# Kernel tuning notes

Measured on AMD Instinct MI355X. Metric: run time of the kernel, lower is better.

## Reference

```python
import jax, jax.numpy as jnp
import numpy as np

B_, D1, D2, M_, Q_, IC, OC, BATCH = 8, 2, 2, 2, 30, 8, 16, 2
BB = 2 * B_            # 16
MM = 2 * (M_ + 1)      # 6
U = 2 * D1 + 1         # 5
V = 2 * D2 + 1         # 5
NC = U * V             # 25


def collect_weights(coeffs):
    # coeffs: [iC, nCoeffs, oC] real -> W: [iC*nCoeffs, oC] complex
    iC, nC, oC = coeffs.shape
    wZ = coeffs[:, 0, :].astype(jnp.complex64)
    wS = coeffs[:, 1:, :].reshape(iC, (nC - 1) // 2, 2, oC).transpose(0, 1, 3, 2)
    w = wS[..., 0] + 1j * wS[..., 1]
    W = jnp.concatenate([jnp.flip(w, 1), wZ[:, None, :], w], axis=1)
    return W.reshape(-1, oC)


def setup_inputs() -> dict:
    key = jax.random.key(0)
    ks = jax.random.split(key, 17)
    r = lambda k, shp, s: (jax.random.normal(k, shp, dtype=jnp.float32) * s)
    return {
        'x_re': r(ks[0], (BATCH, BB, BB, IC), 1.0),
        'x_im': r(ks[1], (BATCH, BB, BB, IC), 1.0),
        'lnAlpha': r(ks[2], (BATCH, BB, BB, IC), 0.3),
        'Phi': r(ks[3], (BATCH, BB, BB, IC), 1.0),
        'lnTau': r(ks[4], (BATCH, BB, BB, IC), 0.3),
        'Psi': r(ks[5], (BATCH, BB, BB, IC), 1.0),
        'pAlpha_re': r(ks[6], (Q_, MM), 0.5),
        'pAlpha_im': r(ks[7], (Q_, MM), 0.5),
        'pPhi_re': r(ks[8], (1, MM), 0.5),
        'pPhi_im': r(ks[9], (1, MM), 0.5),
        'pTau_re': r(ks[10], (Q_, MM, U, 1), 0.5),
        'pTau_im': r(ks[11], (Q_, MM, U, 1), 0.5),
        'pPsi_re': r(ks[12], (1, MM, 1, V), 0.5),
        'pPsi_im': r(ks[13], (1, MM, 1, V), 0.5),
        'F_re': r(ks[14], (Q_, MM, U, V), 1.0),
        'F_im': r(ks[15], (Q_, MM, U, V), 1.0),
        'coeffs': r(ks[16], (IC, NC, OC), 0.1),
    }


def reference(x_re, x_im, lnAlpha, Phi, lnTau, Psi,
              pAlpha_re, pAlpha_im, pPhi_re, pPhi_im,
              pTau_re, pTau_im, pPsi_re, pPsi_im,
              F_re, F_im, coeffs):
    pAlpha = pAlpha_re + 1j * pAlpha_im        # [Q, MM]
    pPhi = pPhi_re + 1j * pPhi_im              # [1, MM]
    pTau = pTau_re + 1j * pTau_im              # [Q, MM, U, 1]
    pPsi = pPsi_re + 1j * pPsi_im              # [1, MM, 1, V]
    F = F_re + 1j * F_im                       # [Q, MM, U, V]
    x = x_re + 1j * x_im                       # [b, BB, BB, iC]
    iC = x.shape[-1]

    # Laplace/Mellin basis on (alpha, phi): [b, Q, MM, BB, BB, iC]
    A = x[:, None, None] * jnp.exp(
        lnAlpha[:, None, None] * pAlpha[None, :, :, None, None, None]
        + Phi[:, None, None] * pPhi[None, :, :, None, None, None])
    # basis on (tau, psi) with filter taps u, v: [b, Q, MM, BB, BB, iC, U, V]
    E = (lnTau[:, None, None, :, :, :, None, None] * pTau[None, :, :, None, None, None]
         + Psi[:, None, None, :, :, :, None, None] * pPsi[None, :, :, None, None, None])
    G = A[..., None, None] * jnp.exp(E)        # [b, Q, MM, BB, BB, iC, U, V]

    W = collect_weights(coeffs)                # [iC*U*V, oC]
    Wr = W.reshape(iC, U, V, -1)               # [iC, U, V, oC]
    # matmul over flattened (iC, u, v), fused with filter F, then permute (0,5,1,2,3,4)
    out = jnp.einsum('bqmyxcuv,qmuv,cuvo->boqmyx', G, F, Wr)
    # return real/imag stacked so the baseline is real-valued: [b, oC, Q, MM, BB, BB, 2]
    return jnp.stack([out.real, out.imag], axis=-1)
```

## Files before the change

kernel.cpp:

```cpp
#include <hip/hip_runtime.h>
#include <hip/hip_bf16.h>

#define NBATCH 2
#define NBB    16
#define NIC    8
#define NOC    16
#define NQ     30
#define NMM    6
#define NU     5
#define NV     5
#define NNC    25

typedef __attribute__((ext_vector_type(8))) short bf16x8;
typedef __attribute__((ext_vector_type(4))) float f32x4;

__device__ __forceinline__ unsigned pk2(float a, float b) {
    unsigned ua = __builtin_bit_cast(unsigned, a);
    unsigned ub = __builtin_bit_cast(unsigned, b);
    ua += 0x7fffu + ((ua >> 16) & 1u);
    ub += 0x7fffu + ((ub >> 16) & 1u);
    return (ua >> 16) | (ub & 0xffff0000u);
}

__device__ __forceinline__ float2 wentry(const float* __restrict__ coeffs,
                                         int c, int n, int o) {
    if (n < 12)
        return make_float2(coeffs[(c * NNC + (23 - 2 * n)) * NOC + o],
                           coeffs[(c * NNC + (24 - 2 * n)) * NOC + o]);
    if (n == 12)
        return make_float2(coeffs[(c * NNC) * NOC + o], 0.0f);
    return make_float2(coeffs[(c * NNC + (2 * n - 25)) * NOC + o],
                       coeffs[(c * NNC + (2 * n - 24)) * NOC + o]);
}

#define EU_G(U)                                                          \
    const float ru##U = __expf(lt * pTau_re[qm * NU + U]);               \
    float su##U, cu##U;                                                  \
    __sincosf(lt * pTau_im[qm * NU + U], &su##U, &cu##U);                \
    const float g##U##r = Are * (ru##U * cu##U) - Aim * (ru##U * su##U); \
    const float g##U##i = Are * (ru##U * su##U) + Aim * (ru##U * cu##U);

#define EVV(V)                                                           \
    const float rv##V = __expf(ps * pPsi_re[m * NV + V]);                \
    float sv##V, cv##V;                                                  \
    __sincosf(ps * pPsi_im[m * NV + V], &sv##V, &cv##V);                 \
    const float e##V##r = rv##V * cv##V, e##V##i = rv##V * sv##V;

#define TAP(N, U, V)                                                     \
    const float tr##N = g##U##r * e##V##r - g##U##i * e##V##i;           \
    const float ti##N = g##U##r * e##V##i + g##U##i * e##V##r;

#define MT_MFMA(SUF, MT, CH, BWR, BWI) {                                 \
    const bf16x8 atr = *reinterpret_cast<const bf16x8*>(                 \
        &T_lds[(CH) * (128 * 36) + ((MT) * 16 + l15) * 36 + sl * 4]);    \
    const bf16x8 ati = *reinterpret_cast<const bf16x8*>(                 \
        &T_lds[(CH) * (128 * 36) + ((MT) * 16 + l15) * 36 + 16 + sl * 4]);\
    aRR##SUF = __builtin_amdgcn_mfma_f32_16x16x32_bf16(atr, BWR, aRR##SUF, 0, 0, 0); \
    aII##SUF = __builtin_amdgcn_mfma_f32_16x16x32_bf16(ati, BWI, aII##SUF, 0, 0, 0); \
    aRI##SUF = __builtin_amdgcn_mfma_f32_16x16x32_bf16(atr, BWI, aRI##SUF, 0, 0, 0); \
    aIR##SUF = __builtin_amdgcn_mfma_f32_16x16x32_bf16(ati, BWR, aIR##SUF, 0, 0, 0); }

__global__ __launch_bounds__(256, 3) void lbc_main(
    const float* __restrict__ x_re,   const float* __restrict__ x_im,
    const float* __restrict__ lnAlpha,const float* __restrict__ Phi,
    const float* __restrict__ lnTau,  const float* __restrict__ Psi,
    const float* __restrict__ pAlpha_re, const float* __restrict__ pAlpha_im,
    const float* __restrict__ pPhi_re,   const float* __restrict__ pPhi_im,
    const float* __restrict__ pTau_re,   const float* __restrict__ pTau_im,
    const float* __restrict__ pPsi_re,   const float* __restrict__ pPsi_im,
    const float* __restrict__ F_re,      const float* __restrict__ F_im,
    const float* __restrict__ coeffs,
    float* __restrict__ out)
{
    __shared__ unsigned T_lds[2 * 128 * 36];
    __shared__ unsigned W_lds[2 * NIC * 64 * 4];

    const int bid  = blockIdx.x;
    const int half = bid & 1;
    const int rest = bid >> 1;
    const int m    = rest % NMM;
    const int q    = (rest / NMM) % NQ;
    const int b    = rest / (NMM * NQ);
    const int qm   = q * NMM + m;

    for (int idx = threadIdx.x; idx < 2 * NIC * 64 * 4; idx += 256) {
        const int j  = idx & 3;
        const int l  = (idx >> 2) & 63;
        const int c  = (idx >> 8) & 7;
        const int pl = idx >> 11;
        const int o  = l & 15;
        const int k0 = (l >> 4) * 8 + 2 * j;
        float v0 = 0.f, v1 = 0.f;
        if (k0 < NNC) {
            const float2 w = wentry(coeffs, c, k0, o);
            const float fr = F_re[qm * NNC + k0], fi = F_im[qm * NNC + k0];
            v0 = pl ? (w.x * fi + w.y * fr) : (w.x * fr - w.y * fi);
        }
        if (k0 + 1 < NNC) {
            const float2 w = wentry(coeffs, c, k0 + 1, o);
            const float fr = F_re[qm * NNC + k0 + 1], fi = F_im[qm * NNC + k0 + 1];
            v1 = pl ? (w.x * fi + w.y * fr) : (w.x * fr - w.y * fi);
        }
        W_lds[idx] = pk2(v0, v1);
    }

    const int tid = threadIdx.x;
    const int ptl = tid & 127;
    const int h   = tid >> 7;
    const int y   = half * 8 + (ptl >> 4);
    const int x   = ptl & 15;
    const int pbase = ((b * NBB + y) * NBB + x) * NIC;

    const int l   = tid & 63;
    const int w   = tid >> 6;
    const int l15 = l & 15;
    const int sl  = l >> 4;

    const float pAre = pAlpha_re[qm], pAim = pAlpha_im[qm];
    const float pPre = pPhi_re[m],    pPim = pPhi_im[m];

    f32x4 aRRa = {0.f, 0.f, 0.f, 0.f}, aIIa = {0.f, 0.f, 0.f, 0.f};
    f32x4 aRIa = {0.f, 0.f, 0.f, 0.f}, aIRa = {0.f, 0.f, 0.f, 0.f};
    f32x4 aRRb = {0.f, 0.f, 0.f, 0.f}, aIIb = {0.f, 0.f, 0.f, 0.f};
    f32x4 aRIb = {0.f, 0.f, 0.f, 0.f}, aIRb = {0.f, 0.f, 0.f, 0.f};

    __syncthreads();

    #pragma unroll 1
    for (int s = 0; s < 4; ++s) {
        {
            const int c  = h * 4 + s;
            const int pc = pbase + c;
            const float xr = x_re[pc], xi = x_im[pc];
            const float la = lnAlpha[pc], ph = Phi[pc];
            const float lt = lnTau[pc],   ps = Psi[pc];

            const float ar = la * pAre + ph * pPre;
            const float ai = la * pAim + ph * pPim;
            const float ea = __expf(ar);
            float sa, ca;
            __sincosf(ai, &sa, &ca);
            const float er_ = ea * ca, ei_ = ea * sa;
            const float Are = xr * er_ - xi * ei_;
            const float Aim = xr * ei_ + xi * er_;

            EU_G(0) EU_G(1) EU_G(2) EU_G(3) EU_G(4)
            EVV(0) EVV(1) EVV(2) EVV(3) EVV(4)

            uint4* trow = reinterpret_cast<uint4*>(&T_lds[h * (128 * 36) + ptl * 36]);

            {
                TAP(0,0,0) TAP(1,0,1) TAP(2,0,2) TAP(3,0,3)
                TAP(4,0,4) TAP(5,1,0) TAP(6,1,1) TAP(7,1,2)
                trow[0] = make_uint4(pk2(tr0,tr1), pk2(tr2,tr3), pk2(tr4,tr5), pk2(tr6,tr7));
                trow[4] = make_uint4(pk2(ti0,ti1), pk2(ti2,ti3), pk2(ti4,ti5), pk2(ti6,ti7));
            }
            {
                TAP(8,1,3) TAP(9,1,4) TAP(10,2,0) TAP(11,2,1)
                TAP(12,2,2) TAP(13,2,3) TAP(14,2,4) TAP(15,3,0)
                trow[1] = make_uint4(pk2(tr8,tr9), pk2(tr10,tr11), pk2(tr12,tr13), pk2(tr14,tr15));
                trow[5] = make_uint4(pk2(ti8,ti9), pk2(ti10,ti11), pk2(ti12,ti13), pk2(ti14,ti15));
            }
            {
                TAP(16,3,1) TAP(17,3,2) TAP(18,3,3) TAP(19,3,4)
                TAP(20,4,0) TAP(21,4,1) TAP(22,4,2) TAP(23,4,3)
                trow[2] = make_uint4(pk2(tr16,tr17), pk2(tr18,tr19), pk2(tr20,tr21), pk2(tr22,tr23));
                trow[6] = make_uint4(pk2(ti16,ti17), pk2(ti18,ti19), pk2(ti20,ti21), pk2(ti22,ti23));
            }
            {
                TAP(24,4,4)
                trow[3] = make_uint4(pk2(tr24, 0.f), 0u, 0u, 0u);
                trow[7] = make_uint4(pk2(ti24, 0.f), 0u, 0u, 0u);
            }
        }
        __syncthreads();

        {
            const int c0 = s;
            const bf16x8 bwr0 = *reinterpret_cast<const bf16x8*>(&W_lds[((0 * NIC + c0) * 64 + l) * 4]);
            const bf16x8 bwi0 = *reinterpret_cast<const bf16x8*>(&W_lds[((1 * NIC + c0) * 64 + l) * 4]);
            MT_MFMA(a, 2 * w,     0, bwr0, bwi0)
            MT_MFMA(b, 2 * w + 1, 0, bwr0, bwi0)

            const int c1 = 4 + s;
            const bf16x8 bwr1 = *reinterpret_cast<const bf16x8*>(&W_lds[((0 * NIC + c1) * 64 + l) * 4]);
            const bf16x8 bwi1 = *reinterpret_cast<const bf16x8*>(&W_lds[((1 * NIC + c1) * 64 + l) * 4]);
            MT_MFMA(a, 2 * w,     1, bwr1, bwi1)
            MT_MFMA(b, 2 * w + 1, 1, bwr1, bwi1)
        }
        __syncthreads();
    }

    const int o = l15;
    const size_t plane = (((size_t)b * NOC + o) * NQ + q) * NMM + m;
    float4* const o4 = reinterpret_cast<float4*>(out);
    {
        const f32x4 vr = aRRa - aIIa;
        const f32x4 vi = aRIa + aIRa;
        const size_t base2 = plane * 256 + half * 128 + (2 * w) * 16 + sl * 4;
        o4[(base2 >> 1)]     = make_float4(vr.x, vi.x, vr.y, vi.y);
        o4[(base2 >> 1) + 1] = make_float4(vr.z, vi.z, vr.w, vi.w);
    }
    {
        const f32x4 vr = aRRb - aIIb;
        const f32x4 vi = aRIb + aIRb;
        const size_t base2 = plane * 256 + half * 128 + (2 * w + 1) * 16 + sl * 4;
        o4[(base2 >> 1)]     = make_float4(vr.x, vi.x, vr.y, vi.y);
        o4[(base2 >> 1) + 1] = make_float4(vr.z, vi.z, vr.w, vi.w);
    }
}

extern "C" void kernel_launch(void* const* d_in, const int* in_sizes, int n_in,
                              void* d_out, int out_size, void* d_ws, size_t ws_size,
                              hipStream_t stream) {
    const float* x_re      = (const float*)d_in[0];
    const float* x_im      = (const float*)d_in[1];
    const float* lnAlpha   = (const float*)d_in[2];
    const float* Phi       = (const float*)d_in[3];
    const float* lnTau     = (const float*)d_in[4];
    const float* Psi       = (const float*)d_in[5];
    const float* pAlpha_re = (const float*)d_in[6];
    const float* pAlpha_im = (const float*)d_in[7];
    const float* pPhi_re   = (const float*)d_in[8];
    const float* pPhi_im   = (const float*)d_in[9];
    const float* pTau_re   = (const float*)d_in[10];
    const float* pTau_im   = (const float*)d_in[11];
    const float* pPsi_re   = (const float*)d_in[12];
    const float* pPsi_im   = (const float*)d_in[13];
    const float* F_re      = (const float*)d_in[14];
    const float* F_im      = (const float*)d_in[15];
    const float* coeffs    = (const float*)d_in[16];
    float* out = (float*)d_out;

    dim3 grid(NBATCH * NQ * NMM * 2);
    dim3 block(256);
    lbc_main<<<grid, block, 0, stream>>>(
        x_re, x_im, lnAlpha, Phi, lnTau, Psi,
        pAlpha_re, pAlpha_im, pPhi_re, pPhi_im,
        pTau_re, pTau_im, pPsi_re, pPsi_im,
        F_re, F_im, coeffs, out);
}
```

Baseline: 115.6 us.

## Vectorize per-point input loads, hoist tau/psi params, overlap first T build with W staging

Each thread now loads its four input channels per array with a single float4 load up front, replacing the scalar per-iteration global loads. The pTau/pPsi parameters are hoisted into registers outside the loop. The first T tile is built before the W staging loop, and the loop is restructured so the last iteration skips a barrier. This is meant to cut global load latency and instruction count inside the loop, at the cost of more live registers under launch bounds of 256 threads with 3 blocks.

Result: faster. 110.1 us (-4.8%).

```diff
diff --git a/kernel.cpp b/kernel.cpp
--- a/kernel.cpp
+++ b/kernel.cpp
@@ -34,21 +34,51 @@
 }
 
 #define EU_G(U)                                                          \
-    const float ru##U = __expf(lt * pTau_re[qm * NU + U]);               \
+    const float ru##U = __expf(lt * pTr##U);                             \
     float su##U, cu##U;                                                  \
-    __sincosf(lt * pTau_im[qm * NU + U], &su##U, &cu##U);                \
+    __sincosf(lt * pTi##U, &su##U, &cu##U);                              \
     const float g##U##r = Are * (ru##U * cu##U) - Aim * (ru##U * su##U); \
     const float g##U##i = Are * (ru##U * su##U) + Aim * (ru##U * cu##U);
 
 #define EVV(V)                                                           \
-    const float rv##V = __expf(ps * pPsi_re[m * NV + V]);                \
+    const float rv##V = __expf(ps * pSr##V);                             \
     float sv##V, cv##V;                                                  \
-    __sincosf(ps * pPsi_im[m * NV + V], &sv##V, &cv##V);                 \
+    __sincosf(ps * pSi##V, &sv##V, &cv##V);                              \
     const float e##V##r = rv##V * cv##V, e##V##i = rv##V * sv##V;
 
 #define TAP(N, U, V)                                                     \
     const float tr##N = g##U##r * e##V##r - g##U##i * e##V##i;           \
     const float ti##N = g##U##r * e##V##i + g##U##i * e##V##r;
+
+#define TBUILD(XR, XI, LA, PH, LT, PS) {                                 \
+    const float xr = (XR), xi = (XI), la = (LA);                         \
+    const float ph = (PH), lt = (LT), ps = (PS);                         \
+    const float ar = la * pAre + ph * pPre;                              \
+    const float ai = la * pAim + ph * pPim;                              \
+    const float ea = __expf(ar);                                         \
+    float sa, ca;                                                        \
+    __sincosf(ai, &sa, &ca);                                             \
+    const float er_ = ea * ca, ei_ = ea * sa;                            \
+    const float Are = xr * er_ - xi * ei_;                               \
+    const float Aim = xr * ei_ + xi * er_;                               \
+    EU_G(0) EU_G(1) EU_G(2) EU_G(3) EU_G(4)                              \
+    EVV(0) EVV(1) EVV(2) EVV(3) EVV(4)                                   \
+    uint4* trow = reinterpret_cast<uint4*>(&T_lds[h * (128 * 36) + ptl * 36]); \
+    {   TAP(0,0,0) TAP(1,0,1) TAP(2,0,2) TAP(3,0,3)                      \
+        TAP(4,0,4) TAP(5,1,0) TAP(6,1,1) TAP(7,1,2)                      \
+        trow[0] = make_uint4(pk2(tr0,tr1), pk2(tr2,tr3), pk2(tr4,tr5), pk2(tr6,tr7));   \
+        trow[4] = make_uint4(pk2(ti0,ti1), pk2(ti2,ti3), pk2(ti4,ti5), pk2(ti6,ti7)); } \
+    {   TAP(8,1,3) TAP(9,1,4) TAP(10,2,0) TAP(11,2,1)                    \
+        TAP(12,2,2) TAP(13,2,3) TAP(14,2,4) TAP(15,3,0)                  \
+        trow[1] = make_uint4(pk2(tr8,tr9), pk2(tr10,tr11), pk2(tr12,tr13), pk2(tr14,tr15)); \
+        trow[5] = make_uint4(pk2(ti8,ti9), pk2(ti10,ti11), pk2(ti12,ti13), pk2(ti14,ti15)); } \
+    {   TAP(16,3,1) TAP(17,3,2) TAP(18,3,3) TAP(19,3,4)                  \
+        TAP(20,4,0) TAP(21,4,1) TAP(22,4,2) TAP(23,4,3)                  \
+        trow[2] = make_uint4(pk2(tr16,tr17), pk2(tr18,tr19), pk2(tr20,tr21), pk2(tr22,tr23)); \
+        trow[6] = make_uint4(pk2(ti16,ti17), pk2(ti18,ti19), pk2(ti20,ti21), pk2(ti22,ti23)); } \
+    {   TAP(24,4,4)                                                      \
+        trow[3] = make_uint4(pk2(tr24, 0.f), 0u, 0u, 0u);                \
+        trow[7] = make_uint4(pk2(ti24, 0.f), 0u, 0u, 0u); } }
 
 #define MT_MFMA(SUF, MT, CH, BWR, BWI) {                                 \
     const bf16x8 atr = *reinterpret_cast<const bf16x8*>(                 \
@@ -83,112 +113,92 @@
     const int b    = rest / (NMM * NQ);
     const int qm   = q * NMM + m;
 
-    for (int idx = threadIdx.x; idx < 2 * NIC * 64 * 4; idx += 256) {
-        const int j  = idx & 3;
-        const int l  = (idx >> 2) & 63;
-        const int c  = (idx >> 8) & 7;
-        const int pl = idx >> 11;
-        const int o  = l & 15;
-        const int k0 = (l >> 4) * 8 + 2 * j;
-        float v0 = 0.f, v1 = 0.f;
-        if (k0 < NNC) {
-            const float2 w = wentry(coeffs, c, k0, o);
-            const float fr = F_re[qm * NNC + k0], fi = F_im[qm * NNC + k0];
-            v0 = pl ? (w.x * fi + w.y * fr) : (w.x * fr - w.y * fi);
-        }
-        if (k0 + 1 < NNC) {
-            const float2 w = wentry(coeffs, c, k0 + 1, o);
-            const float fr = F_re[qm * NNC + k0 + 1], fi = F_im[qm * NNC + k0 + 1];
-            v1 = pl ? (w.x * fi + w.y * fr) : (w.x * fr - w.y * fi);
-        }
-        W_lds[idx] = pk2(v0, v1);
-    }
-
     const int tid = threadIdx.x;
     const int ptl = tid & 127;
     const int h   = tid >> 7;
     const int y   = half * 8 + (ptl >> 4);
     const int x   = ptl & 15;
-    const int pbase = ((b * NBB + y) * NBB + x) * NIC;
+    const int pt  = (b * NBB + y) * NBB + x;
 
     const int l   = tid & 63;
     const int w   = tid >> 6;
     const int l15 = l & 15;
     const int sl  = l >> 4;
 
+    const int p4 = pt * 2 + h;
+    const float4 xr4 = reinterpret_cast<const float4*>(x_re)[p4];
+    const float4 xi4 = reinterpret_cast<const float4*>(x_im)[p4];
+    const float4 la4 = reinterpret_cast<const float4*>(lnAlpha)[p4];
+    const float4 ph4 = reinterpret_cast<const float4*>(Phi)[p4];
+    const float4 lt4 = reinterpret_cast<const float4*>(lnTau)[p4];
+    const float4 ps4 = reinterpret_cast<const float4*>(Psi)[p4];
+
     const float pAre = pAlpha_re[qm], pAim = pAlpha_im[qm];
     const float pPre = pPhi_re[m],    pPim = pPhi_im[m];
-
-    f32x4 aRRa = {0.f, 0.f, 0.f, 0.f}, aIIa = {0.f, 0.f, 0.f, 0.f};
-    f32x4 aRIa = {0.f, 0.f, 0.f, 0.f}, aIRa = {0.f, 0.f, 0.f, 0.f};
-    f32x4 aRRb = {0.f, 0.f, 0.f, 0.f}, aIIb = {0.f, 0.f, 0.f, 0.f};
-    f32x4 aRIb = {0.f, 0.f, 0.f, 0.f}, aIRb = {0.f, 0.f, 0.f, 0.f};
+    const float pTr0 = pTau_re[qm*NU+0], pTi0 = pTau_im[qm*NU+0];
+    const float pTr1 = pTau_re[qm*NU+1], pTi1 = pTau_im[qm*NU+1];
+    const float pTr2 = pTau_re[qm*NU+2], pTi2 = pTau_im[qm*NU+2];
+    const float pTr3 = pTau_re[qm*NU+3], pTi3 = pTau_im[qm*NU+3];
+    const float pTr4 = pTau_re[qm*NU+4], pTi4 = pTau_im[qm*NU+4];
+    const float pSr0 = pPsi_re[m*NV+0],  pSi0 = pPsi_im[m*NV+0];
+    const float pSr1 = pPsi_re[m*NV+1],  pSi1 = pPsi_im[m*NV+1];
+    const float pSr2 = pPsi_re[m*NV+2],  pSi2 = pPsi_im[m*NV+2];
+    const float pSr3 = pPsi_re[m*NV+3],  pSi3 = pPsi_im[m*NV+3];
+    const float pSr4 = pPsi_re[m*NV+4],  pSi4 = pPsi_im[m*NV+4];
+
+    TBUILD(xr4.x, xi4.x, la4.x, ph4.x, lt4.x, ps4.x)
+
+    for (int idx = threadIdx.x; idx < 2 * NIC * 64 * 4; idx += 256) {
+        const int j  = idx & 3;
+        const int ll = (idx >> 2) & 63;
+        const int c  = (idx >> 8) & 7;
+        const int pl = idx >> 11;
+        const int o  = ll & 15;
+        const int k0 = (ll >> 4) * 8 + 2 * j;
+        float v0 = 0.f, v1 = 0.f;
+        if (k0 < NNC) {
+            const float2 wv = wentry(coeffs, c, k0, o);
+            const float fr = F_re[qm * NNC + k0], fi = F_im[qm * NNC + k0];
+            v0 = pl ? (wv.x * fi + wv.y * fr) : (wv.x * fr - wv.y * fi);
+        }
+        if (k0 + 1 < NNC) {
+            const float2 wv = wentry(coeffs, c, k0 + 1, o);
+            const float fr = F_re[qm * NNC + k0 + 1], fi = F_im[qm * NNC + k0 + 1];
+            v1 = pl ? (wv.x * fi + wv.y * fr) : (wv.x * fr - wv.y * fi);
+        }
+        W_lds[idx] = pk2(v0, v1);
+    }
+
+    f32x4 aRRa = {0.f,0.f,0.f,0.f}, aIIa = {0.f,0.f,0.f,0.f};
+    f32x4 aRIa = {0.f,0.f,0.f,0.f}, aIRa = {0.f,0.f,0.f,0.f};
+    f32x4 aRRb = {0.f,0.f,0.f,0.f}, aIIb = {0.f,0.f,0.f,0.f};
+    f32x4 aRIb = {0.f,0.f,0.f,0.f}, aIRb = {0.f,0.f,0.f,0.f};
 
     __syncthreads();
 
     #pragma unroll 1
     for (int s = 0; s < 4; ++s) {
         {
-            const int c  = h * 4 + s;
-            const int pc = pbase + c;
-            const float xr = x_re[pc], xi = x_im[pc];
-            const float la = lnAlpha[pc], ph = Phi[pc];
-            const float lt = lnTau[pc],   ps = Psi[pc];
-
-            const float ar = la * pAre + ph * pPre;
-            const float ai = la * pAim + ph * pPim;
-            const float ea = __expf(ar);
-            float sa, ca;
-            __sincosf(ai, &sa, &ca);
-            const float er_ = ea * ca, ei_ = ea * sa;
-            const float Are = xr * er_ - xi * ei_;
-            const float Aim = xr * ei_ + xi * er_;
-
-            EU_G(0) EU_G(1) EU_G(2) EU_G(3) EU_G(4)
-            EVV(0) EVV(1) EVV(2) EVV(3) EVV(4)
-
-            uint4* trow = reinterpret_cast<uint4*>(&T_lds[h * (128 * 36) + ptl * 36]);
-
-            {
-                TAP(0,0,0) TAP(1,0,1) TAP(2,0,2) TAP(3,0,3)
-                TAP(4,0,4) TAP(5,1,0) TAP(6,1,1) TAP(7,1,2)
-                trow[0] = make_uint4(pk2(tr0,tr1), pk2(tr2,tr3), pk2(tr4,tr5), pk2(tr6,tr7));
-                trow[4] = make_uint4(pk2(ti0,ti1), pk2(ti2,ti3), pk2(ti4,ti5), pk2(ti6,ti7));
-            }
-            {
-                TAP(8,1,3) TAP(9,1,4) TAP(10,2,0) TAP(11,2,1)
-                TAP(12,2,2) TAP(13,2,3) TAP(14,2,4) TAP(15,3,0)
-                trow[1] = make_uint4(pk2(tr8,tr9), pk2(tr10,tr11), pk2(tr12,tr13), pk2(tr14,tr15));
-                trow[5] = make_uint4(pk2(ti8,ti9), pk2(ti10,ti11), pk2(ti12,ti13), pk2(ti14,ti15));
-            }
-            {
-                TAP(16,3,1) TAP(17,3,2) TAP(18,3,3) TAP(19,3,4)
-                TAP(20,4,0) TAP(21,4,1) TAP(22,4,2) TAP(23,4,3)
-                trow[2] = make_uint4(pk2(tr16,tr17), pk2(tr18,tr19), pk2(tr20,tr21), pk2(tr22,tr23));
-                trow[6] = make_uint4(pk2(ti16,ti17), pk2(ti18,ti19), pk2(ti20,ti21), pk2(ti22,ti23));
-            }
-            {
-                TAP(24,4,4)
-                trow[3] = make_uint4(pk2(tr24, 0.f), 0u, 0u, 0u);
-                trow[7] = make_uint4(pk2(ti24, 0.f), 0u, 0u, 0u);
-            }
-        }
-        __syncthreads();
-
-        {
-            const int c0 = s;
-            const bf16x8 bwr0 = *reinterpret_cast<const bf16x8*>(&W_lds[((0 * NIC + c0) * 64 + l) * 4]);
-            const bf16x8 bwi0 = *reinterpret_cast<const bf16x8*>(&W_lds[((1 * NIC + c0) * 64 + l) * 4]);
+            const bf16x8 bwr0 = *reinterpret_cast<const bf16x8*>(&W_lds[((0 * NIC + s) * 64 + l) * 4]);
+            const bf16x8 bwi0 = *reinterpret_cast<const bf16x8*>(&W_lds[((1 * NIC + s) * 64 + l) * 4]);
             MT_MFMA(a, 2 * w,     0, bwr0, bwi0)
             MT_MFMA(b, 2 * w + 1, 0, bwr0, bwi0)
-
-            const int c1 = 4 + s;
-            const bf16x8 bwr1 = *reinterpret_cast<const bf16x8*>(&W_lds[((0 * NIC + c1) * 64 + l) * 4]);
-            const bf16x8 bwi1 = *reinterpret_cast<const bf16x8*>(&W_lds[((1 * NIC + c1) * 64 + l) * 4]);
+            const bf16x8 bwr1 = *reinterpret_cast<const bf16x8*>(&W_lds[((0 * NIC + 4 + s) * 64 + l) * 4]);
+            const bf16x8 bwi1 = *reinterpret_cast<const bf16x8*>(&W_lds[((1 * NIC + 4 + s) * 64 + l) * 4]);
             MT_MFMA(a, 2 * w,     1, bwr1, bwi1)
             MT_MFMA(b, 2 * w + 1, 1, bwr1, bwi1)
         }
-        __syncthreads();
+        if (s < 3) {
+            __syncthreads();
+            const float nxr = s == 0 ? xr4.y : (s == 1 ? xr4.z : xr4.w);
+            const float nxi = s == 0 ? xi4.y : (s == 1 ? xi4.z : xi4.w);
+            const float nla = s == 0 ? la4.y : (s == 1 ? la4.z : la4.w);
+            const float nph = s == 0 ? ph4.y : (s == 1 ? ph4.z : ph4.w);
+            const float nlt = s == 0 ? lt4.y : (s == 1 ? lt4.z : lt4.w);
+            const float nps = s == 0 ? ps4.y : (s == 1 ? ps4.z : ps4.w);
+            TBUILD(nxr, nxi, nla, nph, nlt, nps)
+            __syncthreads();
+        }
     }
 
     const int o = l15;
```
